# Kernel tuning notes

Hardware: AMD Instinct MI355X
Metric: run time of the kernel (lower is better)

## Reference

```python
import jax, jax.numpy as jnp
import numpy as np

L = 0.05  # lx = ly = lz box half-extent

# 8 box corners [8,3]
_CORNERS = jnp.array([[sx * L, sy * L, sz * L]
                      for sx in (-1.0, 1.0) for sy in (-1.0, 1.0) for sz in (-1.0, 1.0)],
                     dtype=jnp.float32)
# match original ordering: [-,-,-],[-,-,+],[-,+,-],... which the comprehension above yields


def _euler_R(pose):
    """pose: [B,6] -> R [B,3,3], t [B,3] (yaw, pitch, roll convention from source)."""
    yaw, pitch, roll = pose[:, 0], pose[:, 1], pose[:, 2]
    cy, sy = jnp.cos(yaw), jnp.sin(yaw)
    cp, sp = jnp.cos(pitch), jnp.sin(pitch)
    cr, sr = jnp.cos(roll), jnp.sin(roll)
    R = jnp.stack([
        jnp.stack([cy * cp, cy * sp * sr - sy * cr, cy * sp * cr + sy * sr], axis=-1),
        jnp.stack([sy * cp, sy * sp * sr + cy * cr, sy * sp * cr - cy * sr], axis=-1),
        jnp.stack([-sp, cp * sr, cp * cr], axis=-1),
    ], axis=-2)  # [B,3,3]
    t = pose[:, 3:]  # [B,3]
    return R, t


def _transform_corners(pose):
    R, t = _euler_R(pose)
    # [B,8,3] = corners @ R^T + t
    return jnp.einsum('bij,nj->bni', R, _CORNERS) + t[:, None, :]


def setup_inputs() -> dict:
    key = jax.random.key(0)
    k1, k2, k3, k4 = jax.random.split(key, 4)
    B, C = 1048576, 16
    return {
        'pred_pose': jax.random.normal(k1, (B, 6), dtype=jnp.float32),
        'pred_class': jax.random.normal(k2, (B, C), dtype=jnp.float32),
        'target_pose': jax.random.normal(k3, (B, 6), dtype=jnp.float32),
        'target_class': jax.random.normal(k4, (B, C), dtype=jnp.float32),
    }


def reference(pred_pose, pred_class, target_pose, target_class):
    pts_pred = _transform_corners(pred_pose)    # [B,8,3]
    pts_gt = _transform_corners(target_pose)    # [B,8,3]
    # per-sample pose diff: mean over 8 corner L2 norms, then mean over batch
    norms = jnp.linalg.norm(pts_pred - pts_gt, axis=-1)  # [B,8]
    loss_pose = norms.mean(axis=-1).mean()
    class_loss = jnp.mean((pred_class - target_class) ** 2)
    total_loss = loss_pose + class_loss
    return total_loss, loss_pose, class_loss
```

## Files before the change

### kernel.cpp

```cpp
#include <hip/hip_runtime.h>
#include <math.h>

#define CORNER_L 0.05f

typedef float f4 __attribute__((ext_vector_type(4)));

constexpr int THREADS = 256;
constexpr int GROUPS  = 1024;
constexpr int CQ = 3, PQ = 2;
constexpr int CBLOCKS = CQ * GROUPS;
constexpr int PBLOCKS = PQ * GROUPS;
constexpr int TOTAL_BLOCKS = CBLOCKS + PBLOCKS;

__device__ __forceinline__ float pose_elem(
    float py, float pp_, float pr, float ptx, float pty, float ptz,
    float ty, float tp_, float tr, float ttx, float tty, float ttz)
{
    float sy1 = __sinf(py),  cy1 = __cosf(py);
    float sp1 = __sinf(pp_), cp1 = __cosf(pp_);
    float sr1 = __sinf(pr),  cr1 = __cosf(pr);
    float sy2 = __sinf(ty),  cy2 = __cosf(ty);
    float sp2 = __sinf(tp_), cp2 = __cosf(tp_);
    float sr2 = __sinf(tr),  cr2 = __cosf(tr);

    float a0 = CORNER_L * (cy1 * cp1 - cy2 * cp2);
    float a1 = CORNER_L * ((cy1 * sp1 * sr1 - sy1 * cr1) - (cy2 * sp2 * sr2 - sy2 * cr2));
    float a2 = CORNER_L * ((cy1 * sp1 * cr1 + sy1 * sr1) - (cy2 * sp2 * cr2 + sy2 * sr2));
    float b0 = CORNER_L * (sy1 * cp1 - sy2 * cp2);
    float b1 = CORNER_L * ((sy1 * sp1 * sr1 + cy1 * cr1) - (sy2 * sp2 * sr2 + cy2 * cr2));
    float b2 = CORNER_L * ((sy1 * sp1 * cr1 - cy1 * sr1) - (sy2 * sp2 * cr2 - cy2 * sr2));
    float c0 = CORNER_L * (sp2 - sp1);
    float c1 = CORNER_L * (cp1 * sr1 - cp2 * sr2);
    float c2 = CORNER_L * (cp1 * cr1 - cp2 * cr2);
    float dtx = ptx - ttx;
    float dty = pty - tty;
    float dtz = ptz - ttz;

    float nsum = 0.0f;
    #pragma unroll
    for (int s = 0; s < 8; ++s) {
        float sx = (s & 4) ? 1.0f : -1.0f;
        float sy = (s & 2) ? 1.0f : -1.0f;
        float sz = (s & 1) ? 1.0f : -1.0f;
        float d0 = sx * a0 + sy * a1 + sz * a2 + dtx;
        float d1 = sx * b0 + sy * b1 + sz * b2 + dty;
        float d2 = sx * c0 + sy * c1 + sz * c2 + dtz;
        nsum += __builtin_amdgcn_sqrtf(d0 * d0 + d1 * d1 + d2 * d2);
    }
    return nsum;
}

__global__ __launch_bounds__(THREADS) void pose_loss_fused(
    const f4* __restrict__ pp4, const f4* __restrict__ pc4,
    const f4* __restrict__ tp4, const f4* __restrict__ tc4,
    float* __restrict__ ws, int n4)
{
    const int tid = threadIdx.x;
    const int g   = blockIdx.x;
    const int grp = g / 5;
    const int r   = g - grp * 5;

    float acc = 0.0f;
    int out_idx;

    if (r < CQ) {
        const int cb = grp * CQ + r;
        const size_t G = (size_t)CBLOCKS * THREADS;
        for (size_t i = (size_t)cb * THREADS + tid; i < (size_t)n4; i += G) {
            f4 p = __builtin_nontemporal_load(pc4 + i);
            f4 t = __builtin_nontemporal_load(tc4 + i);
            f4 d = p - t;
            acc += d.x * d.x + d.y * d.y + d.z * d.z + d.w * d.w;
        }
        out_idx = cb;
    } else {
        const int pb = grp * PQ + (r - CQ);
        const size_t gtid = (size_t)pb * THREADS + tid;
        const size_t f = gtid * 3;
        f4 P0 = __builtin_nontemporal_load(pp4 + f);
        f4 P1 = __builtin_nontemporal_load(pp4 + f + 1);
        f4 P2 = __builtin_nontemporal_load(pp4 + f + 2);
        f4 T0 = __builtin_nontemporal_load(tp4 + f);
        f4 T1 = __builtin_nontemporal_load(tp4 + f + 1);
        f4 T2 = __builtin_nontemporal_load(tp4 + f + 2);
        acc += pose_elem(P0.x, P0.y, P0.z, P0.w, P1.x, P1.y,
                         T0.x, T0.y, T0.z, T0.w, T1.x, T1.y);
        acc += pose_elem(P1.z, P1.w, P2.x, P2.y, P2.z, P2.w,
                         T1.z, T1.w, T2.x, T2.y, T2.z, T2.w);
        out_idx = CBLOCKS + pb;
    }

    #pragma unroll
    for (int off = 32; off > 0; off >>= 1) acc += __shfl_down(acc, off);
    __shared__ float red[4];
    const int lane = tid & 63, wave = tid >> 6;
    if (lane == 0) red[wave] = acc;
    __syncthreads();
    if (tid == 0) ws[out_idx] = red[0] + red[1] + red[2] + red[3];
}

__global__ __launch_bounds__(THREADS) void pose_loss_finalize(
    const float* __restrict__ ws, float* __restrict__ out,
    float inv_pose, float inv_class)
{
    float c = 0.0f, p = 0.0f;
    for (int k = threadIdx.x; k < CBLOCKS; k += THREADS) c += ws[k];
    for (int k = threadIdx.x; k < PBLOCKS; k += THREADS) p += ws[CBLOCKS + k];
    #pragma unroll
    for (int off = 32; off > 0; off >>= 1) {
        p += __shfl_down(p, off);
        c += __shfl_down(c, off);
    }
    __shared__ float r_p[4], r_c[4];
    const int lane = threadIdx.x & 63, wave = threadIdx.x >> 6;
    if (lane == 0) { r_p[wave] = p; r_c[wave] = c; }
    __syncthreads();
    if (threadIdx.x == 0) {
        float lp = (r_p[0] + r_p[1] + r_p[2] + r_p[3]) * inv_pose;
        float lc = (r_c[0] + r_c[1] + r_c[2] + r_c[3]) * inv_class;
        out[0] = lp + lc;
        out[1] = lp;
        out[2] = lc;
    }
}

extern "C" void kernel_launch(void* const* d_in, const int* in_sizes, int n_in,
                              void* d_out, int out_size, void* d_ws, size_t ws_size,
                              hipStream_t stream) {
    const f4* pred_pose    = (const f4*)d_in[0];
    const f4* pred_class   = (const f4*)d_in[1];
    const f4* target_pose  = (const f4*)d_in[2];
    const f4* target_class = (const f4*)d_in[3];
    float* out = (float*)d_out;
    float* ws  = (float*)d_ws;

    const int B  = in_sizes[0] / 6;
    const int n4 = B * 4;

    pose_loss_fused<<<TOTAL_BLOCKS, THREADS, 0, stream>>>(
        pred_pose, pred_class, target_pose, target_class, ws, n4);

    const float inv_pose  = 1.0f / (8.0f  * (float)B);
    const float inv_class = 1.0f / (16.0f * (float)B);
    pose_loss_finalize<<<1, THREADS, 0, stream>>>(ws, out, inv_pose, inv_class);
}
```

Baseline: 173.6 us.

## Fuse class and pose work into every block to overlap loads with trig math

Each block now does both the pose work (two samples per thread) and a fixed eight-trip loop over the class arrays, instead of splitting blocks into class-only and pose-only roles. The pose math is placed between the class-load batches so transcendental compute can hide memory latency within each wave. The grid drops from 5120 to 2048 blocks and writes two partial sums per block. The bounds are hard-coded for B=1048576 (n4/G = 8 trips, gtid*2 covers B), so other sizes would be handled incorrectly.

```diff
diff --git a/kernel.cpp b/kernel.cpp
--- a/kernel.cpp
+++ b/kernel.cpp
@@ -6,11 +6,8 @@
 typedef float f4 __attribute__((ext_vector_type(4)));
 
 constexpr int THREADS = 256;
-constexpr int GROUPS  = 1024;
-constexpr int CQ = 3, PQ = 2;
-constexpr int CBLOCKS = CQ * GROUPS;
-constexpr int PBLOCKS = PQ * GROUPS;
-constexpr int TOTAL_BLOCKS = CBLOCKS + PBLOCKS;
+constexpr int BLOCKS  = 2048;
+constexpr int CTRIPS  = 8;
 
 __device__ __forceinline__ float pose_elem(
     float py, float pp_, float pr, float ptx, float pty, float ptz,
@@ -53,50 +50,61 @@
 __global__ __launch_bounds__(THREADS) void pose_loss_fused(
     const f4* __restrict__ pp4, const f4* __restrict__ pc4,
     const f4* __restrict__ tp4, const f4* __restrict__ tc4,
-    float* __restrict__ ws, int n4)
+    float* __restrict__ ws)
 {
     const int tid = threadIdx.x;
-    const int g   = blockIdx.x;
-    const int grp = g / 5;
-    const int r   = g - grp * 5;
+    const int b   = blockIdx.x;
+    const size_t gtid = (size_t)b * THREADS + tid;
+    constexpr size_t G = (size_t)BLOCKS * THREADS;
 
-    float acc = 0.0f;
-    int out_idx;
+    const size_t f = gtid * 3;
+    f4 P0 = __builtin_nontemporal_load(pp4 + f);
+    f4 P1 = __builtin_nontemporal_load(pp4 + f + 1);
+    f4 P2 = __builtin_nontemporal_load(pp4 + f + 2);
+    f4 T0 = __builtin_nontemporal_load(tp4 + f);
+    f4 T1 = __builtin_nontemporal_load(tp4 + f + 1);
+    f4 T2 = __builtin_nontemporal_load(tp4 + f + 2);
 
-    if (r < CQ) {
-        const int cb = grp * CQ + r;
-        const size_t G = (size_t)CBLOCKS * THREADS;
-        for (size_t i = (size_t)cb * THREADS + tid; i < (size_t)n4; i += G) {
-            f4 p = __builtin_nontemporal_load(pc4 + i);
-            f4 t = __builtin_nontemporal_load(tc4 + i);
-            f4 d = p - t;
-            acc += d.x * d.x + d.y * d.y + d.z * d.z + d.w * d.w;
-        }
-        out_idx = cb;
-    } else {
-        const int pb = grp * PQ + (r - CQ);
-        const size_t gtid = (size_t)pb * THREADS + tid;
-        const size_t f = gtid * 3;
-        f4 P0 = __builtin_nontemporal_load(pp4 + f);
-        f4 P1 = __builtin_nontemporal_load(pp4 + f + 1);
-        f4 P2 = __builtin_nontemporal_load(pp4 + f + 2);
-        f4 T0 = __builtin_nontemporal_load(tp4 + f);
-        f4 T1 = __builtin_nontemporal_load(tp4 + f + 1);
-        f4 T2 = __builtin_nontemporal_load(tp4 + f + 2);
-        acc += pose_elem(P0.x, P0.y, P0.z, P0.w, P1.x, P1.y,
-                         T0.x, T0.y, T0.z, T0.w, T1.x, T1.y);
-        acc += pose_elem(P1.z, P1.w, P2.x, P2.y, P2.z, P2.w,
-                         T1.z, T1.w, T2.x, T2.y, T2.z, T2.w);
-        out_idx = CBLOCKS + pb;
+    float accc = 0.0f;
+    float accp = 0.0f;
+
+    #pragma unroll 2
+    for (int k = 0; k < CTRIPS / 2; ++k) {
+        const size_t i = gtid + (size_t)k * G;
+        f4 p = __builtin_nontemporal_load(pc4 + i);
+        f4 t = __builtin_nontemporal_load(tc4 + i);
+        f4 d = p - t;
+        accc += d.x * d.x + d.y * d.y + d.z * d.z + d.w * d.w;
     }
 
+    accp += pose_elem(P0.x, P0.y, P0.z, P0.w, P1.x, P1.y,
+                      T0.x, T0.y, T0.z, T0.w, T1.x, T1.y);
+
+    #pragma unroll 2
+    for (int k = CTRIPS / 2; k < CTRIPS; ++k) {
+        const size_t i = gtid + (size_t)k * G;
+        f4 p = __builtin_nontemporal_load(pc4 + i);
+        f4 t = __builtin_nontemporal_load(tc4 + i);
+        f4 d = p - t;
+        accc += d.x * d.x + d.y * d.y + d.z * d.z + d.w * d.w;
+    }
+
+    accp += pose_elem(P1.z, P1.w, P2.x, P2.y, P2.z, P2.w,
+                      T1.z, T1.w, T2.x, T2.y, T2.z, T2.w);
+
     #pragma unroll
-    for (int off = 32; off > 0; off >>= 1) acc += __shfl_down(acc, off);
-    __shared__ float red[4];
+    for (int off = 32; off > 0; off >>= 1) {
+        accc += __shfl_down(accc, off);
+        accp += __shfl_down(accp, off);
+    }
+    __shared__ float red_c[4], red_p[4];
     const int lane = tid & 63, wave = tid >> 6;
-    if (lane == 0) red[wave] = acc;
+    if (lane == 0) { red_c[wave] = accc; red_p[wave] = accp; }
     __syncthreads();
-    if (tid == 0) ws[out_idx] = red[0] + red[1] + red[2] + red[3];
+    if (tid == 0) {
+        ws[b]          = red_c[0] + red_c[1] + red_c[2] + red_c[3];
+        ws[BLOCKS + b] = red_p[0] + red_p[1] + red_p[2] + red_p[3];
+    }
 }
 
 __global__ __launch_bounds__(THREADS) void pose_loss_finalize(
@@ -104,8 +112,10 @@
     float inv_pose, float inv_class)
 {
     float c = 0.0f, p = 0.0f;
-    for (int k = threadIdx.x; k < CBLOCKS; k += THREADS) c += ws[k];
-    for (int k = threadIdx.x; k < PBLOCKS; k += THREADS) p += ws[CBLOCKS + k];
+    for (int k = threadIdx.x; k < BLOCKS; k += THREADS) {
+        c += ws[k];
+        p += ws[BLOCKS + k];
+    }
     #pragma unroll
     for (int off = 32; off > 0; off >>= 1) {
         p += __shfl_down(p, off);
@@ -134,11 +144,10 @@
     float* out = (float*)d_out;
     float* ws  = (float*)d_ws;
 
-    const int B  = in_sizes[0] / 6;
-    const int n4 = B * 4;
+    const int B = in_sizes[0] / 6;
 
-    pose_loss_fused<<<TOTAL_BLOCKS, THREADS, 0, stream>>>(
-        pred_pose, pred_class, target_pose, target_class, ws, n4);
+    pose_loss_fused<<<BLOCKS, THREADS, 0, stream>>>(
+        pred_pose, pred_class, target_pose, target_class, ws);
 
     const float inv_pose  = 1.0f / (8.0f  * (float)B);
     const float inv_class = 1.0f / (16.0f * (float)B);
```

After: 174.2 us. About the same (+0.3%).
